# Kernel optimization log

Hardware: AMD Instinct MI355X
Metric: run time of the kernel (lower is better)

The kernel has to match this reference:

```python
import jax, jax.numpy as jnp
import numpy as np

HID = 256


def _mlp(h, ws, bs):
    # 4-layer MLP: tanh x3, sigmoid output (matches nn.Sequential in torch code)
    h = jnp.tanh(h @ ws[0] + bs[0])
    h = jnp.tanh(h @ ws[1] + bs[1])
    h = jnp.tanh(h @ ws[2] + bs[2])
    return jax.nn.sigmoid(h @ ws[3] + bs[3])


def setup_inputs() -> dict:
    key = jax.random.key(0)
    N, K, DE = 100000, 32, 8
    IN1 = K * DE          # 256
    MID = 5
    IN2 = K * MID         # 160
    E = N * K
    ks = jax.random.split(key, 20)
    x = jax.random.normal(ks[0], (N, DE), dtype=jnp.float32)
    edge_index = jax.random.randint(ks[1], (2, E), 0, N, dtype=jnp.int64)
    edge_attr = jax.random.normal(ks[2], (E, DE), dtype=jnp.float32)

    def lin(k, fan_in, fan_out):
        kw, kb = jax.random.split(k)
        lim = 1.0 / np.sqrt(fan_in)
        w = jax.random.uniform(kw, (fan_in, fan_out), jnp.float32, -lim, lim)
        b = jax.random.uniform(kb, (fan_out,), jnp.float32, -lim, lim)
        return w, b

    dims1 = [(IN1, HID), (HID, HID), (HID, HID), (HID, MID)]
    dims2 = [(IN2, HID), (HID, HID), (HID, HID), (HID, 1)]
    inp = {"x": x, "edge_index": edge_index, "edge_attr": edge_attr}
    for i, (fi, fo) in enumerate(dims1):
        w, b = lin(ks[3 + i], fi, fo)
        inp[f"w1_{i}"], inp[f"b1_{i}"] = w, b
    for i, (fi, fo) in enumerate(dims2):
        w, b = lin(ks[10 + i], fi, fo)
        inp[f"w2_{i}"], inp[f"b2_{i}"] = w, b
    return inp


def reference(x, edge_index, edge_attr,
              w1_0, b1_0, w1_1, b1_1, w1_2, b1_2, w1_3, b1_3,
              w2_0, b2_0, w2_1, b2_1, w2_2, b2_2, w2_3, b2_3):
    K = 32
    IN1 = w1_0.shape[0]              # 256
    MID = w1_3.shape[1]              # 5
    # GNN1: message = edge_attr; aggregate reshapes to [N, IN1] then MLP -> [N, MID]
    out1 = _mlp(edge_attr.reshape(-1, IN1), (w1_0, w1_1, w1_2, w1_3), (b1_0, b1_1, b1_2, b1_3))
    # GNN2: message = x_j = out1[edge_index[1]] (flow='target_to_source')
    gathered = out1[edge_index[1]]                     # [E, MID] irregular gather
    out2 = _mlp(gathered.reshape(-1, K * MID), (w2_0, w2_1, w2_2, w2_3), (b2_0, b2_1, b2_2, b2_3))
    return out2[:, 0]                                  # squeeze dim 1 -> [N]
```

## Files before the change

kernel.cpp:

```cpp
#include <hip/hip_runtime.h>
#include <stdint.h>

typedef uint16_t u16;
typedef uint32_t u32;
typedef __attribute__((ext_vector_type(8)))  __bf16 bf16x8;
typedef __attribute__((ext_vector_type(16))) float  f32x16;

#define NROWS   100000
#define E_EDGES 3200000

#define HIDX(r, g) (((r) << 8) + ((((g) ^ ((r) & 31))) << 3))

#define MFMA(a, b, c) __builtin_amdgcn_mfma_f32_32x32x16_bf16((a), (b), (c), 0, 0, 0)

__device__ __forceinline__ u32 pk_bf16(float a, float b) {
    u32 ua = __builtin_bit_cast(u32, a), ub = __builtin_bit_cast(u32, b);
    ua = (ua + 0x7FFFu + ((ua >> 16) & 1u)) >> 16;
    ub = (ub + 0x7FFFu + ((ub >> 16) & 1u)) >> 16;
    return ua | (ub << 16);
}
__device__ __forceinline__ float fast_tanh(float x) {
    float e = __expf(2.0f * x);
    return 1.0f - __fdividef(2.0f, e + 1.0f);
}
__device__ __forceinline__ float fast_sigmoid(float x) {
    return __fdividef(1.0f, 1.0f + __expf(-x));
}

__device__ __forceinline__ void dense256_reg(u16* Hs, const u16* __restrict__ WB,
                                             const float* __restrict__ bias,
                                             int wave, int lane) {
    const int l31 = lane & 31, lh = lane >> 5;
    const int nt0 = (wave & 3) * 2;
    const int bb  = (wave >> 2) * 2;
    const int rb0 = bb * 32 + l31, rb1 = rb0 + 32;

    f32x16 acc[4];
#pragma unroll
    for (int i = 0; i < 4; ++i)
#pragma unroll
        for (int j = 0; j < 16; ++j) acc[i][j] = 0.0f;

    __syncthreads();

    const u16* wbase = WB + (nt0 * 32 + l31) * 16 + lh * 8;
#pragma unroll
    for (int c = 0; c < 8; ++c) {
#pragma unroll
        for (int ks = 0; ks < 2; ++ks) {
            const int g = c * 4 + ks * 2 + lh;
            bf16x8 w0 = *(const bf16x8*)(wbase + c * 8192 + ks * 4096);
            bf16x8 w1 = *(const bf16x8*)(wbase + c * 8192 + ks * 4096 + 512);
            bf16x8 h0 = *(const bf16x8*)(Hs + HIDX(rb0, g));
            bf16x8 h1 = *(const bf16x8*)(Hs + HIDX(rb1, g));
            acc[0] = MFMA(w0, h0, acc[0]);
            acc[1] = MFMA(w0, h1, acc[1]);
            acc[2] = MFMA(w1, h0, acc[2]);
            acc[3] = MFMA(w1, h1, acc[3]);
        }
    }
    __syncthreads();

#pragma unroll
    for (int i = 0; i < 2; ++i) {
        const int nt = nt0 + i;
#pragma unroll
        for (int rg = 0; rg < 4; ++rg) {
            const int ns = nt * 32 + rg * 8 + lh * 4;
            const float4 bv = *(const float4*)(bias + ns);
#pragma unroll
            for (int b = 0; b < 2; ++b) {
                f32x16& A = acc[i * 2 + b];
                float x0 = fast_tanh(A[rg * 4 + 0] + bv.x);
                float x1 = fast_tanh(A[rg * 4 + 1] + bv.y);
                float x2 = fast_tanh(A[rg * 4 + 2] + bv.z);
                float x3 = fast_tanh(A[rg * 4 + 3] + bv.w);
                const int r = (bb + b) * 32 + l31;
                const int g = nt * 4 + rg;
                uint2 v; v.x = pk_bf16(x0, x1); v.y = pk_bf16(x2, x3);
                *(uint2*)(Hs + (r << 8) + (((g) ^ (r & 31)) << 3) + lh * 4) = v;
            }
        }
    }
}

__device__ __forceinline__ f32x16 final_dense_reg(const u16* Hs, const u16* __restrict__ WBf,
                                                  int wave, int lane) {
    const int l31 = lane & 31, lh = lane >> 5;
    __syncthreads();
    f32x16 acc;
#pragma unroll
    for (int j = 0; j < 16; ++j) acc[j] = 0.0f;
    if (wave < 4) {
        const u16* wbase = WBf + l31 * 16 + lh * 8;
#pragma unroll
        for (int c = 0; c < 8; ++c)
#pragma unroll
            for (int ks = 0; ks < 2; ++ks) {
                bf16x8 w = *(const bf16x8*)(wbase + (c * 2 + ks) * 512);
                const int g = c * 4 + ks * 2 + lh;
                bf16x8 h = *(const bf16x8*)(Hs + HIDX(wave * 32 + l31, g));
                acc = MFMA(w, h, acc);
            }
    }
    return acc;
}

__global__ __launch_bounds__(512, 4) void mlp1_kernel(
    const float* __restrict__ ea, const u16* __restrict__ WB1, const u16* __restrict__ WB13,
    const float* __restrict__ b0, const float* __restrict__ b1, const float* __restrict__ b2,
    const float* __restrict__ b3, u16* __restrict__ out1) {
    __shared__ u16 Hs[128 * 256];
    const int tid = threadIdx.x, wave = tid >> 6, lane = tid & 63, blk = blockIdx.x;

#pragma unroll
    for (int i = 0; i < 8; ++i) {
        const int r = i * 16 + (tid >> 5);
        const int g = tid & 31;
        const int rg_ = blk * 128 + r;
        if (rg_ < NROWS) {
            const float* p = ea + (size_t)rg_ * 256 + g * 8;
            float4 a0 = *(const float4*)p;
            float4 a1 = *(const float4*)(p + 4);
            uint4 v; v.x = pk_bf16(a0.x, a0.y); v.y = pk_bf16(a0.z, a0.w);
            v.z = pk_bf16(a1.x, a1.y); v.w = pk_bf16(a1.z, a1.w);
            *(uint4*)(Hs + HIDX(r, g)) = v;
        }
    }
    dense256_reg(Hs, WB1,          b0, wave, lane);
    dense256_reg(Hs, WB1 + 65536,  b1, wave, lane);
    dense256_reg(Hs, WB1 + 131072, b2, wave, lane);
    f32x16 acc = final_dense_reg(Hs, WB13, wave, lane);

    if (wave < 4) {
        const int row_g = blk * 128 + wave * 32 + (lane & 31);
        if (row_g < NROWS) {
            if ((lane >> 5) == 0) {
                float s0 = fast_sigmoid(acc[0] + b3[0]);
                float s1 = fast_sigmoid(acc[1] + b3[1]);
                float s2 = fast_sigmoid(acc[2] + b3[2]);
                float s3 = fast_sigmoid(acc[3] + b3[3]);
                uint2 v; v.x = pk_bf16(s0, s1); v.y = pk_bf16(s2, s3);
                *(uint2*)(out1 + (size_t)row_g * 8) = v;
            } else {
                float s4 = fast_sigmoid(acc[0] + b3[4]);
                uint2 v; v.x = pk_bf16(s4, 0.0f); v.y = 0u;
                *(uint2*)(out1 + (size_t)row_g * 8 + 4) = v;
            }
        }
    }
}

__global__ __launch_bounds__(512, 4) void mlp2_kernel(
    const int* __restrict__ idx1, const u16* __restrict__ out1,
    const u16* __restrict__ WB2, const u16* __restrict__ WB23,
    const float* __restrict__ b0, const float* __restrict__ b1, const float* __restrict__ b2,
    const float* __restrict__ b3, float* __restrict__ out) {
    __shared__ u16 Hs[128 * 256];
    const int tid = threadIdx.x, wave = tid >> 6, lane = tid & 63, blk = blockIdx.x;

    int nodes[8];
#pragma unroll
    for (int i = 0; i < 8; ++i) {
        const long e = (long)blk * 4096 + i * 512 + tid;
        nodes[i] = (e < (long)E_EDGES) ? idx1[e] : 0;
    }
#pragma unroll
    for (int i = 0; i < 8; ++i) {
        const int li = i * 512 + tid;
        const int r = li >> 5, j = li & 31;
        const long e = (long)blk * 4096 + li;
        if (e < (long)E_EDGES) {
            uint4 v = *(const uint4*)(out1 + (size_t)nodes[i] * 8);
            *(uint4*)(Hs + HIDX(r, j)) = v;
        }
    }
    dense256_reg(Hs, WB2,          b0, wave, lane);
    dense256_reg(Hs, WB2 + 65536,  b1, wave, lane);
    dense256_reg(Hs, WB2 + 131072, b2, wave, lane);
    f32x16 acc = final_dense_reg(Hs, WB23, wave, lane);

    if (wave < 4) {
        const int row_g = blk * 128 + wave * 32 + (lane & 31);
        if (row_g < NROWS && (lane >> 5) == 0)
            out[row_g] = fast_sigmoid(acc[0] + b3[0]);
    }
}

__global__ void transform_kernel(
    const float* __restrict__ w10, const float* __restrict__ w11, const float* __restrict__ w12,
    const float* __restrict__ w13, const float* __restrict__ w20, const float* __restrict__ w21,
    const float* __restrict__ w22, const float* __restrict__ w23, u16* __restrict__ ws) {
    const int id = blockIdx.x * 256 + threadIdx.x;
    float val;
    if (id < 196608) {
        int layer = id >> 16, rem = id & 65535;
        int c = rem >> 13, s = (rem >> 12) & 1, n = (rem >> 4) & 255, kl = rem & 15;
        int k = c * 32 + s * 16 + kl;
        const float* w = layer == 0 ? w10 : (layer == 1 ? w11 : w12);
        val = w[k * 256 + n];
    } else if (id < 204800) {
        int rem = id - 196608;
        int c = rem >> 10, s = (rem >> 9) & 1, n = (rem >> 4) & 31, kl = rem & 15;
        int k = c * 32 + s * 16 + kl;
        val = (n < 5) ? w13[k * 5 + n] : 0.0f;
    } else if (id < 401408) {
        int rem = id - 204800;
        int layer = rem >> 16; rem &= 65535;
        int c = rem >> 13, s = (rem >> 12) & 1, n = (rem >> 4) & 255, kl = rem & 15;
        int k = c * 32 + s * 16 + kl;
        if (layer == 0) {
            int j = k >> 3, v = k & 7;
            val = (v < 5) ? w20[(j * 5 + v) * 256 + n] : 0.0f;
        } else {
            val = (layer == 1 ? w21 : w22)[k * 256 + n];
        }
    } else {
        int rem = id - 401408;
        int c = rem >> 10, s = (rem >> 9) & 1, n = (rem >> 4) & 31, kl = rem & 15;
        int k = c * 32 + s * 16 + kl;
        val = (n == 0) ? w23[k] : 0.0f;
    }
    u32 u = __builtin_bit_cast(u32, val);
    u = (u + 0x7FFFu + ((u >> 16) & 1u)) >> 16;
    ws[id] = (u16)u;
}

extern "C" void kernel_launch(void* const* d_in, const int* in_sizes, int n_in,
                              void* d_out, int out_size, void* d_ws, size_t ws_size,
                              hipStream_t stream) {
    const int*   ei  = (const int*)d_in[1];
    const float* ea  = (const float*)d_in[2];
    const float* w10 = (const float*)d_in[3];  const float* b10 = (const float*)d_in[4];
    const float* w11 = (const float*)d_in[5];  const float* b11 = (const float*)d_in[6];
    const float* w12 = (const float*)d_in[7];  const float* b12 = (const float*)d_in[8];
    const float* w13 = (const float*)d_in[9];  const float* b13 = (const float*)d_in[10];
    const float* w20 = (const float*)d_in[11]; const float* b20 = (const float*)d_in[12];
    const float* w21 = (const float*)d_in[13]; const float* b21 = (const float*)d_in[14];
    const float* w22 = (const float*)d_in[15]; const float* b22 = (const float*)d_in[16];
    const float* w23 = (const float*)d_in[17]; const float* b23 = (const float*)d_in[18];

    u16* ws   = (u16*)d_ws;
    u16* WB1  = ws;
    u16* WB13 = ws + 196608;
    u16* WB2  = ws + 204800;
    u16* WB23 = ws + 401408;
    u16* out1 = ws + 409600;

    hipLaunchKernelGGL(transform_kernel, dim3(1600), dim3(256), 0, stream,
                       w10, w11, w12, w13, w20, w21, w22, w23, ws);
    hipLaunchKernelGGL(mlp1_kernel, dim3(782), dim3(512), 0, stream,
                       ea, WB1, WB13, b10, b11, b12, b13, out1);
    hipLaunchKernelGGL(mlp2_kernel, dim3(782), dim3(512), 0, stream,
                       ei + E_EDGES, out1, WB2, WB23, b20, b21, b22, b23, (float*)d_out);
}
```

Before: 396.0 us.

## Hold weight slices in registers, prefetch next layer, double-buffer activations in LDS

Each of the 8 waves now owns one 32-column output tile. It keeps its 16 weight fragments for the current layer in registers and overwrites them with the next layer's weights while the MFMA loop runs. Block row count drops from 128 to 64, with ping-pong LDS buffers H0/H1, so each layer needs one barrier instead of two and the grid doubles. This hides global weight-load latency behind compute and gives more blocks for occupancy. The cost is more register pressure and twice as many weight reads across blocks.

```diff
diff --git a/kernel.cpp b/kernel.cpp
--- a/kernel.cpp
+++ b/kernel.cpp
@@ -27,81 +27,59 @@
     return __fdividef(1.0f, 1.0f + __expf(-x));
 }
 
-__device__ __forceinline__ void dense256_reg(u16* Hs, const u16* __restrict__ WB,
-                                             const float* __restrict__ bias,
-                                             int wave, int lane) {
-    const int l31 = lane & 31, lh = lane >> 5;
-    const int nt0 = (wave & 3) * 2;
-    const int bb  = (wave >> 2) * 2;
-    const int rb0 = bb * 32 + l31, rb1 = rb0 + 32;
-
-    f32x16 acc[4];
-#pragma unroll
-    for (int i = 0; i < 4; ++i)
-#pragma unroll
-        for (int j = 0; j < 16; ++j) acc[i][j] = 0.0f;
-
-    __syncthreads();
-
-    const u16* wbase = WB + (nt0 * 32 + l31) * 16 + lh * 8;
-#pragma unroll
-    for (int c = 0; c < 8; ++c) {
-#pragma unroll
-        for (int ks = 0; ks < 2; ++ks) {
-            const int g = c * 4 + ks * 2 + lh;
-            bf16x8 w0 = *(const bf16x8*)(wbase + c * 8192 + ks * 4096);
-            bf16x8 w1 = *(const bf16x8*)(wbase + c * 8192 + ks * 4096 + 512);
-            bf16x8 h0 = *(const bf16x8*)(Hs + HIDX(rb0, g));
-            bf16x8 h1 = *(const bf16x8*)(Hs + HIDX(rb1, g));
-            acc[0] = MFMA(w0, h0, acc[0]);
-            acc[1] = MFMA(w0, h1, acc[1]);
-            acc[2] = MFMA(w1, h0, acc[2]);
-            acc[3] = MFMA(w1, h1, acc[3]);
-        }
-    }
-    __syncthreads();
-
-#pragma unroll
-    for (int i = 0; i < 2; ++i) {
-        const int nt = nt0 + i;
-#pragma unroll
-        for (int rg = 0; rg < 4; ++rg) {
-            const int ns = nt * 32 + rg * 8 + lh * 4;
-            const float4 bv = *(const float4*)(bias + ns);
-#pragma unroll
-            for (int b = 0; b < 2; ++b) {
-                f32x16& A = acc[i * 2 + b];
-                float x0 = fast_tanh(A[rg * 4 + 0] + bv.x);
-                float x1 = fast_tanh(A[rg * 4 + 1] + bv.y);
-                float x2 = fast_tanh(A[rg * 4 + 2] + bv.z);
-                float x3 = fast_tanh(A[rg * 4 + 3] + bv.w);
-                const int r = (bb + b) * 32 + l31;
-                const int g = nt * 4 + rg;
-                uint2 v; v.x = pk_bf16(x0, x1); v.y = pk_bf16(x2, x3);
-                *(uint2*)(Hs + (r << 8) + (((g) ^ (r & 31)) << 3) + lh * 4) = v;
-            }
-        }
-    }
-}
-
-__device__ __forceinline__ f32x16 final_dense_reg(const u16* Hs, const u16* __restrict__ WBf,
-                                                  int wave, int lane) {
-    const int l31 = lane & 31, lh = lane >> 5;
-    __syncthreads();
+__device__ __forceinline__ void load_w16(bf16x8 (&W)[16], const u16* __restrict__ base,
+                                         int stride) {
+#pragma unroll
+    for (int s = 0; s < 16; ++s) W[s] = *(const bf16x8*)(base + s * stride);
+}
+
+__device__ __forceinline__ void dense_layer(const u16* __restrict__ Hin, u16* __restrict__ Hout,
+                                            bf16x8 (&W)[16], const u16* __restrict__ pfbase,
+                                            int pfstride, const float* __restrict__ bias,
+                                            int nt, int l31, int lh) {
+    f32x16 acc0, acc1;
+#pragma unroll
+    for (int j = 0; j < 16; ++j) { acc0[j] = 0.0f; acc1[j] = 0.0f; }
+
+#pragma unroll
+    for (int s = 0; s < 16; ++s) {
+        const int g = 2 * s + lh;
+        bf16x8 h0 = *(const bf16x8*)(Hin + HIDX(l31, g));
+        bf16x8 h1 = *(const bf16x8*)(Hin + HIDX(32 + l31, g));
+        acc0 = MFMA(W[s], h0, acc0);
+        acc1 = MFMA(W[s], h1, acc1);
+        W[s] = *(const bf16x8*)(pfbase + s * pfstride);
+    }
+#pragma unroll
+    for (int rg = 0; rg < 4; ++rg) {
+        const float4 bv = *(const float4*)(bias + nt * 32 + rg * 8 + lh * 4);
+#pragma unroll
+        for (int b = 0; b < 2; ++b) {
+            const f32x16& A = b ? acc1 : acc0;
+            float x0 = fast_tanh(A[rg * 4 + 0] + bv.x);
+            float x1 = fast_tanh(A[rg * 4 + 1] + bv.y);
+            float x2 = fast_tanh(A[rg * 4 + 2] + bv.z);
+            float x3 = fast_tanh(A[rg * 4 + 3] + bv.w);
+            const int r = b * 32 + l31;
+            const int g = nt * 4 + rg;
+            uint2 v; v.x = pk_bf16(x0, x1); v.y = pk_bf16(x2, x3);
+            *(uint2*)(Hout + (r << 8) + (((g) ^ (r & 31)) << 3) + lh * 4) = v;
+        }
+    }
+}
+
+__device__ __forceinline__ f32x16 final_dense(const u16* __restrict__ Hin, bf16x8 (&W)[16],
+                                              int wave, int l31, int lh) {
     f32x16 acc;
 #pragma unroll
     for (int j = 0; j < 16; ++j) acc[j] = 0.0f;
-    if (wave < 4) {
-        const u16* wbase = WBf + l31 * 16 + lh * 8;
-#pragma unroll
-        for (int c = 0; c < 8; ++c)
-#pragma unroll
-            for (int ks = 0; ks < 2; ++ks) {
-                bf16x8 w = *(const bf16x8*)(wbase + (c * 2 + ks) * 512);
-                const int g = c * 4 + ks * 2 + lh;
-                bf16x8 h = *(const bf16x8*)(Hs + HIDX(wave * 32 + l31, g));
-                acc = MFMA(w, h, acc);
-            }
+    if (wave < 2) {
+#pragma unroll
+        for (int s = 0; s < 16; ++s) {
+            const int g = 2 * s + lh;
+            bf16x8 h = *(const bf16x8*)(Hin + HIDX(wave * 32 + l31, g));
+            acc = MFMA(W[s], h, acc);
+        }
     }
     return acc;
 }
@@ -110,32 +88,43 @@
     const float* __restrict__ ea, const u16* __restrict__ WB1, const u16* __restrict__ WB13,
     const float* __restrict__ b0, const float* __restrict__ b1, const float* __restrict__ b2,
     const float* __restrict__ b3, u16* __restrict__ out1) {
-    __shared__ u16 Hs[128 * 256];
+    __shared__ u16 H0[64 * 256];
+    __shared__ u16 H1[64 * 256];
     const int tid = threadIdx.x, wave = tid >> 6, lane = tid & 63, blk = blockIdx.x;
-
-#pragma unroll
-    for (int i = 0; i < 8; ++i) {
+    const int l31 = lane & 31, lh = lane >> 5, nt = wave;
+    const int woff = (nt * 32 + l31) * 16 + lh * 8;
+
+    bf16x8 W[16];
+    load_w16(W, WB1 + woff, 4096);
+
+#pragma unroll
+    for (int i = 0; i < 4; ++i) {
         const int r = i * 16 + (tid >> 5);
         const int g = tid & 31;
-        const int rg_ = blk * 128 + r;
+        const int rg_ = blk * 64 + r;
+        uint4 v = {0u, 0u, 0u, 0u};
         if (rg_ < NROWS) {
             const float* p = ea + (size_t)rg_ * 256 + g * 8;
             float4 a0 = *(const float4*)p;
             float4 a1 = *(const float4*)(p + 4);
-            uint4 v; v.x = pk_bf16(a0.x, a0.y); v.y = pk_bf16(a0.z, a0.w);
+            v.x = pk_bf16(a0.x, a0.y); v.y = pk_bf16(a0.z, a0.w);
             v.z = pk_bf16(a1.x, a1.y); v.w = pk_bf16(a1.z, a1.w);
-            *(uint4*)(Hs + HIDX(r, g)) = v;
-        }
-    }
-    dense256_reg(Hs, WB1,          b0, wave, lane);
-    dense256_reg(Hs, WB1 + 65536,  b1, wave, lane);
-    dense256_reg(Hs, WB1 + 131072, b2, wave, lane);
-    f32x16 acc = final_dense_reg(Hs, WB13, wave, lane);
-
-    if (wave < 4) {
-        const int row_g = blk * 128 + wave * 32 + (lane & 31);
+        }
+        *(uint4*)(H0 + HIDX(r, g)) = v;
+    }
+    __syncthreads();
+    dense_layer(H0, H1, W, WB1 + 65536  + woff, 4096, b0, nt, l31, lh);
+    __syncthreads();
+    dense_layer(H1, H0, W, WB1 + 131072 + woff, 4096, b1, nt, l31, lh);
+    __syncthreads();
+    dense_layer(H0, H1, W, WB13 + l31 * 16 + lh * 8, 512, b2, nt, l31, lh);
+    __syncthreads();
+    f32x16 acc = final_dense(H1, W, wave, l31, lh);
+
+    if (wave < 2) {
+        const int row_g = blk * 64 + wave * 32 + l31;
         if (row_g < NROWS) {
-            if ((lane >> 5) == 0) {
+            if (lh == 0) {
                 float s0 = fast_sigmoid(acc[0] + b3[0]);
                 float s1 = fast_sigmoid(acc[1] + b3[1]);
                 float s2 = fast_sigmoid(acc[2] + b3[2]);
@@ -156,33 +145,41 @@
     const u16* __restrict__ WB2, const u16* __restrict__ WB23,
     const float* __restrict__ b0, const float* __restrict__ b1, const float* __restrict__ b2,
     const float* __restrict__ b3, float* __restrict__ out) {
-    __shared__ u16 Hs[128 * 256];
+    __shared__ u16 H0[64 * 256];
+    __shared__ u16 H1[64 * 256];
     const int tid = threadIdx.x, wave = tid >> 6, lane = tid & 63, blk = blockIdx.x;
-
-    int nodes[8];
-#pragma unroll
-    for (int i = 0; i < 8; ++i) {
-        const long e = (long)blk * 4096 + i * 512 + tid;
-        nodes[i] = (e < (long)E_EDGES) ? idx1[e] : 0;
-    }
-#pragma unroll
-    for (int i = 0; i < 8; ++i) {
+    const int l31 = lane & 31, lh = lane >> 5, nt = wave;
+    const int woff = (nt * 32 + l31) * 16 + lh * 8;
+
+    bf16x8 W[16];
+    load_w16(W, WB2 + woff, 4096);
+
+    int nodes[4];
+#pragma unroll
+    for (int i = 0; i < 4; ++i) {
+        const long e = (long)blk * 2048 + i * 512 + tid;
+        nodes[i] = (e < (long)E_EDGES) ? idx1[e] : -1;
+    }
+#pragma unroll
+    for (int i = 0; i < 4; ++i) {
         const int li = i * 512 + tid;
         const int r = li >> 5, j = li & 31;
-        const long e = (long)blk * 4096 + li;
-        if (e < (long)E_EDGES) {
-            uint4 v = *(const uint4*)(out1 + (size_t)nodes[i] * 8);
-            *(uint4*)(Hs + HIDX(r, j)) = v;
-        }
-    }
-    dense256_reg(Hs, WB2,          b0, wave, lane);
-    dense256_reg(Hs, WB2 + 65536,  b1, wave, lane);
-    dense256_reg(Hs, WB2 + 131072, b2, wave, lane);
-    f32x16 acc = final_dense_reg(Hs, WB23, wave, lane);
-
-    if (wave < 4) {
-        const int row_g = blk * 128 + wave * 32 + (lane & 31);
-        if (row_g < NROWS && (lane >> 5) == 0)
+        uint4 v = {0u, 0u, 0u, 0u};
+        if (nodes[i] >= 0) v = *(const uint4*)(out1 + (size_t)nodes[i] * 8);
+        *(uint4*)(H0 + HIDX(r, j)) = v;
+    }
+    __syncthreads();
+    dense_layer(H0, H1, W, WB2 + 65536  + woff, 4096, b0, nt, l31, lh);
+    __syncthreads();
+    dense_layer(H1, H0, W, WB2 + 131072 + woff, 4096, b1, nt, l31, lh);
+    __syncthreads();
+    dense_layer(H0, H1, W, WB23 + l31 * 16 + lh * 8, 512, b2, nt, l31, lh);
+    __syncthreads();
+    f32x16 acc = final_dense(H1, W, wave, l31, lh);
+
+    if (wave < 2) {
+        const int row_g = blk * 64 + wave * 32 + l31;
+        if (row_g < NROWS && lh == 0)
             out[row_g] = fast_sigmoid(acc[0] + b3[0]);
     }
 }
@@ -249,8 +246,8 @@
 
     hipLaunchKernelGGL(transform_kernel, dim3(1600), dim3(256), 0, stream,
                        w10, w11, w12, w13, w20, w21, w22, w23, ws);
-    hipLaunchKernelGGL(mlp1_kernel, dim3(782), dim3(512), 0, stream,
+    hipLaunchKernelGGL(mlp1_kernel, dim3(1563), dim3(512), 0, stream,
                        ea, WB1, WB13, b10, b11, b12, b13, out1);
-    hipLaunchKernelGGL(mlp2_kernel, dim3(782), dim3(512), 0, stream,
+    hipLaunchKernelGGL(mlp2_kernel, dim3(1563), dim3(512), 0, stream,
                        ei + E_EDGES, out1, WB2, WB23, b20, b21, b22, b23, (float*)d_out);
 }
```

Measured after the change: 364.2 us. -8.0%, faster.

## Shrink row tile to 64 with 4-wave blocks, software-pipeline MFMA loads

Applied to the files above, without the earlier changes.

Blocks now handle 64 rows with 256 threads instead of 128 rows with 512. Each wave computes 64 output columns for all 64 rows, so the weight layout is reordered to a plain K-step stride. The MFMA inner loop double-buffers its weight and LDS operand loads so they overlap the previous step's MFMAs. tanh and sigmoid now use the hardware exp2 and rcp builtins. The smaller tile halves LDS use and raises grid size, which should improve occupancy and load balance. The cost is that each weight fragment is reused across fewer rows.

```diff
diff --git a/kernel.cpp b/kernel.cpp
--- a/kernel.cpp
+++ b/kernel.cpp
@@ -13,28 +13,25 @@
 
 #define MFMA(a, b, c) __builtin_amdgcn_mfma_f32_32x32x16_bf16((a), (b), (c), 0, 0, 0)
 
-__device__ __forceinline__ u32 pk_bf16(float a, float b) {
+__device__ __forceinline__ u32 pk2(float a, float b) {
     u32 ua = __builtin_bit_cast(u32, a), ub = __builtin_bit_cast(u32, b);
     ua = (ua + 0x7FFFu + ((ua >> 16) & 1u)) >> 16;
     ub = (ub + 0x7FFFu + ((ub >> 16) & 1u)) >> 16;
     return ua | (ub << 16);
 }
 __device__ __forceinline__ float fast_tanh(float x) {
-    float e = __expf(2.0f * x);
-    return 1.0f - __fdividef(2.0f, e + 1.0f);
+    float e = __builtin_amdgcn_exp2f(x * 2.885390081777927f);
+    float r = __builtin_amdgcn_rcpf(e + 1.0f);
+    return __builtin_fmaf(-2.0f, r, 1.0f);
 }
 __device__ __forceinline__ float fast_sigmoid(float x) {
-    return __fdividef(1.0f, 1.0f + __expf(-x));
-}
-
-__device__ __forceinline__ void dense256_reg(u16* Hs, const u16* __restrict__ WB,
-                                             const float* __restrict__ bias,
-                                             int wave, int lane) {
-    const int l31 = lane & 31, lh = lane >> 5;
-    const int nt0 = (wave & 3) * 2;
-    const int bb  = (wave >> 2) * 2;
-    const int rb0 = bb * 32 + l31, rb1 = rb0 + 32;
-
+    float e = __builtin_amdgcn_exp2f(x * -1.4426950408889634f);
+    return __builtin_amdgcn_rcpf(1.0f + e);
+}
+
+__device__ __forceinline__ void dense256(u16* __restrict__ Hs, const u16* __restrict__ WB,
+                                         const float* __restrict__ bias,
+                                         int wave, int l31, int lh) {
     f32x16 acc[4];
 #pragma unroll
     for (int i = 0; i < 4; ++i)
@@ -43,146 +40,155 @@
 
     __syncthreads();
 
-    const u16* wbase = WB + (nt0 * 32 + l31) * 16 + lh * 8;
-#pragma unroll
-    for (int c = 0; c < 8; ++c) {
-#pragma unroll
-        for (int ks = 0; ks < 2; ++ks) {
-            const int g = c * 4 + ks * 2 + lh;
-            bf16x8 w0 = *(const bf16x8*)(wbase + c * 8192 + ks * 4096);
-            bf16x8 w1 = *(const bf16x8*)(wbase + c * 8192 + ks * 4096 + 512);
-            bf16x8 h0 = *(const bf16x8*)(Hs + HIDX(rb0, g));
-            bf16x8 h1 = *(const bf16x8*)(Hs + HIDX(rb1, g));
-            acc[0] = MFMA(w0, h0, acc[0]);
-            acc[1] = MFMA(w0, h1, acc[1]);
-            acc[2] = MFMA(w1, h0, acc[2]);
-            acc[3] = MFMA(w1, h1, acc[3]);
-        }
+    const u16* wp = WB + (wave * 64 + l31) * 16 + lh * 8;
+    bf16x8 w0 = *(const bf16x8*)(wp);
+    bf16x8 w1 = *(const bf16x8*)(wp + 512);
+    bf16x8 h0 = *(const bf16x8*)(Hs + HIDX(l31, lh));
+    bf16x8 h1 = *(const bf16x8*)(Hs + HIDX(32 + l31, lh));
+
+#pragma unroll
+    for (int s = 0; s < 16; ++s) {
+        bf16x8 nw0 = w0, nw1 = w1, nh0 = h0, nh1 = h1;
+        if (s < 15) {
+            const int ng = 2 * (s + 1) + lh;
+            nw0 = *(const bf16x8*)(wp + (s + 1) * 4096);
+            nw1 = *(const bf16x8*)(wp + (s + 1) * 4096 + 512);
+            nh0 = *(const bf16x8*)(Hs + HIDX(l31, ng));
+            nh1 = *(const bf16x8*)(Hs + HIDX(32 + l31, ng));
+        }
+        acc[0] = MFMA(w0, h0, acc[0]);
+        acc[1] = MFMA(w0, h1, acc[1]);
+        acc[2] = MFMA(w1, h0, acc[2]);
+        acc[3] = MFMA(w1, h1, acc[3]);
+        w0 = nw0; w1 = nw1; h0 = nh0; h1 = nh1;
     }
     __syncthreads();
 
 #pragma unroll
     for (int i = 0; i < 2; ++i) {
-        const int nt = nt0 + i;
+        const int nt = wave * 2 + i;
 #pragma unroll
         for (int rg = 0; rg < 4; ++rg) {
-            const int ns = nt * 32 + rg * 8 + lh * 4;
-            const float4 bv = *(const float4*)(bias + ns);
+            const float4 bv = *(const float4*)(bias + nt * 32 + rg * 8 + lh * 4);
 #pragma unroll
             for (int b = 0; b < 2; ++b) {
-                f32x16& A = acc[i * 2 + b];
+                const f32x16& A = acc[i * 2 + b];
                 float x0 = fast_tanh(A[rg * 4 + 0] + bv.x);
                 float x1 = fast_tanh(A[rg * 4 + 1] + bv.y);
                 float x2 = fast_tanh(A[rg * 4 + 2] + bv.z);
                 float x3 = fast_tanh(A[rg * 4 + 3] + bv.w);
-                const int r = (bb + b) * 32 + l31;
+                const int r = b * 32 + l31;
                 const int g = nt * 4 + rg;
-                uint2 v; v.x = pk_bf16(x0, x1); v.y = pk_bf16(x2, x3);
+                uint2 v; v.x = pk2(x0, x1); v.y = pk2(x2, x3);
                 *(uint2*)(Hs + (r << 8) + (((g) ^ (r & 31)) << 3) + lh * 4) = v;
             }
         }
     }
 }
 
-__device__ __forceinline__ f32x16 final_dense_reg(const u16* Hs, const u16* __restrict__ WBf,
-                                                  int wave, int lane) {
-    const int l31 = lane & 31, lh = lane >> 5;
+__device__ __forceinline__ f32x16 final_dense(const u16* __restrict__ Hs,
+                                              const u16* __restrict__ WBf,
+                                              int wave, int l31, int lh) {
     __syncthreads();
     f32x16 acc;
 #pragma unroll
     for (int j = 0; j < 16; ++j) acc[j] = 0.0f;
-    if (wave < 4) {
-        const u16* wbase = WBf + l31 * 16 + lh * 8;
-#pragma unroll
-        for (int c = 0; c < 8; ++c)
-#pragma unroll
-            for (int ks = 0; ks < 2; ++ks) {
-                bf16x8 w = *(const bf16x8*)(wbase + (c * 2 + ks) * 512);
-                const int g = c * 4 + ks * 2 + lh;
-                bf16x8 h = *(const bf16x8*)(Hs + HIDX(wave * 32 + l31, g));
-                acc = MFMA(w, h, acc);
+    if (wave < 2) {
+        const u16* wp = WBf + l31 * 16 + lh * 8;
+        bf16x8 w = *(const bf16x8*)(wp);
+        bf16x8 h = *(const bf16x8*)(Hs + HIDX(wave * 32 + l31, lh));
+#pragma unroll
+        for (int s = 0; s < 16; ++s) {
+            bf16x8 nw = w, nh = h;
+            if (s < 15) {
+                nw = *(const bf16x8*)(wp + (s + 1) * 512);
+                nh = *(const bf16x8*)(Hs + HIDX(wave * 32 + l31, 2 * (s + 1) + lh));
             }
+            acc = MFMA(w, h, acc);
+            w = nw; h = nh;
+        }
     }
     return acc;
 }
 
-__global__ __launch_bounds__(512, 4) void mlp1_kernel(
+__global__ __launch_bounds__(256, 4) void mlp1_kernel(
     const float* __restrict__ ea, const u16* __restrict__ WB1, const u16* __restrict__ WB13,
     const float* __restrict__ b0, const float* __restrict__ b1, const float* __restrict__ b2,
     const float* __restrict__ b3, u16* __restrict__ out1) {
-    __shared__ u16 Hs[128 * 256];
+    __shared__ u16 Hs[64 * 256];
     const int tid = threadIdx.x, wave = tid >> 6, lane = tid & 63, blk = blockIdx.x;
+    const int l31 = lane & 31, lh = lane >> 5;
 
 #pragma unroll
     for (int i = 0; i < 8; ++i) {
-        const int r = i * 16 + (tid >> 5);
-        const int g = tid & 31;
-        const int rg_ = blk * 128 + r;
+        const int li = i * 256 + tid;
+        const int r = li >> 5, g = li & 31;
+        const int rg_ = blk * 64 + r;
+        uint4 v = {0u, 0u, 0u, 0u};
         if (rg_ < NROWS) {
             const float* p = ea + (size_t)rg_ * 256 + g * 8;
             float4 a0 = *(const float4*)p;
             float4 a1 = *(const float4*)(p + 4);
-            uint4 v; v.x = pk_bf16(a0.x, a0.y); v.y = pk_bf16(a0.z, a0.w);
-            v.z = pk_bf16(a1.x, a1.y); v.w = pk_bf16(a1.z, a1.w);
-            *(uint4*)(Hs + HIDX(r, g)) = v;
-        }
-    }
-    dense256_reg(Hs, WB1,          b0, wave, lane);
-    dense256_reg(Hs, WB1 + 65536,  b1, wave, lane);
-    dense256_reg(Hs, WB1 + 131072, b2, wave, lane);
-    f32x16 acc = final_dense_reg(Hs, WB13, wave, lane);
-
-    if (wave < 4) {
-        const int row_g = blk * 128 + wave * 32 + (lane & 31);
+            v.x = pk2(a0.x, a0.y); v.y = pk2(a0.z, a0.w);
+            v.z = pk2(a1.x, a1.y); v.w = pk2(a1.z, a1.w);
+        }
+        *(uint4*)(Hs + HIDX(r, g)) = v;
+    }
+    dense256(Hs, WB1,          b0, wave, l31, lh);
+    dense256(Hs, WB1 + 65536,  b1, wave, l31, lh);
+    dense256(Hs, WB1 + 131072, b2, wave, l31, lh);
+    f32x16 acc = final_dense(Hs, WB13, wave, l31, lh);
+
+    if (wave < 2) {
+        const int row_g = blk * 64 + wave * 32 + l31;
         if (row_g < NROWS) {
-            if ((lane >> 5) == 0) {
+            if (lh == 0) {
                 float s0 = fast_sigmoid(acc[0] + b3[0]);
                 float s1 = fast_sigmoid(acc[1] + b3[1]);
                 float s2 = fast_sigmoid(acc[2] + b3[2]);
                 float s3 = fast_sigmoid(acc[3] + b3[3]);
-                uint2 v; v.x = pk_bf16(s0, s1); v.y = pk_bf16(s2, s3);
+                uint2 v; v.x = pk2(s0, s1); v.y = pk2(s2, s3);
                 *(uint2*)(out1 + (size_t)row_g * 8) = v;
             } else {
                 float s4 = fast_sigmoid(acc[0] + b3[4]);
-                uint2 v; v.x = pk_bf16(s4, 0.0f); v.y = 0u;
+                uint2 v; v.x = pk2(s4, 0.0f); v.y = 0u;
                 *(uint2*)(out1 + (size_t)row_g * 8 + 4) = v;
             }
         }
     }
 }
 
-__global__ __launch_bounds__(512, 4) void mlp2_kernel(
+__global__ __launch_bounds__(256, 4) void mlp2_kernel(
     const int* __restrict__ idx1, const u16* __restrict__ out1,
     const u16* __restrict__ WB2, const u16* __restrict__ WB23,
     const float* __restrict__ b0, const float* __restrict__ b1, const float* __restrict__ b2,
     const float* __restrict__ b3, float* __restrict__ out) {
-    __shared__ u16 Hs[128 * 256];
+    __shared__ u16 Hs[64 * 256];
     const int tid = threadIdx.x, wave = tid >> 6, lane = tid & 63, blk = blockIdx.x;
+    const int l31 = lane & 31, lh = lane >> 5;
 
     int nodes[8];
 #pragma unroll
     for (int i = 0; i < 8; ++i) {
-        const long e = (long)blk * 4096 + i * 512 + tid;
-        nodes[i] = (e < (long)E_EDGES) ? idx1[e] : 0;
+        const long e = (long)blk * 2048 + i * 256 + tid;
+        nodes[i] = (e < (long)E_EDGES) ? idx1[e] : -1;
     }
 #pragma unroll
     for (int i = 0; i < 8; ++i) {
-        const int li = i * 512 + tid;
+        const int li = i * 256 + tid;
         const int r = li >> 5, j = li & 31;
-        const long e = (long)blk * 4096 + li;
-        if (e < (long)E_EDGES) {
-            uint4 v = *(const uint4*)(out1 + (size_t)nodes[i] * 8);
-            *(uint4*)(Hs + HIDX(r, j)) = v;
-        }
-    }
-    dense256_reg(Hs, WB2,          b0, wave, lane);
-    dense256_reg(Hs, WB2 + 65536,  b1, wave, lane);
-    dense256_reg(Hs, WB2 + 131072, b2, wave, lane);
-    f32x16 acc = final_dense_reg(Hs, WB23, wave, lane);
-
-    if (wave < 4) {
-        const int row_g = blk * 128 + wave * 32 + (lane & 31);
-        if (row_g < NROWS && (lane >> 5) == 0)
+        uint4 v = {0u, 0u, 0u, 0u};
+        if (nodes[i] >= 0) v = *(const uint4*)(out1 + (size_t)nodes[i] * 8);
+        *(uint4*)(Hs + HIDX(r, j)) = v;
+    }
+    dense256(Hs, WB2,          b0, wave, l31, lh);
+    dense256(Hs, WB2 + 65536,  b1, wave, l31, lh);
+    dense256(Hs, WB2 + 131072, b2, wave, l31, lh);
+    f32x16 acc = final_dense(Hs, WB23, wave, l31, lh);
+
+    if (wave < 2) {
+        const int row_g = blk * 64 + wave * 32 + l31;
+        if (row_g < NROWS && lh == 0)
             out[row_g] = fast_sigmoid(acc[0] + b3[0]);
     }
 }
@@ -195,20 +201,20 @@
     float val;
     if (id < 196608) {
         int layer = id >> 16, rem = id & 65535;
-        int c = rem >> 13, s = (rem >> 12) & 1, n = (rem >> 4) & 255, kl = rem & 15;
-        int k = c * 32 + s * 16 + kl;
+        int s = rem >> 12, n = (rem >> 4) & 255, kl = rem & 15;
+        int k = s * 16 + kl;
         const float* w = layer == 0 ? w10 : (layer == 1 ? w11 : w12);
         val = w[k * 256 + n];
     } else if (id < 204800) {
         int rem = id - 196608;
-        int c = rem >> 10, s = (rem >> 9) & 1, n = (rem >> 4) & 31, kl = rem & 15;
-        int k = c * 32 + s * 16 + kl;
+        int s = rem >> 9, n = (rem >> 4) & 31, kl = rem & 15;
+        int k = s * 16 + kl;
         val = (n < 5) ? w13[k * 5 + n] : 0.0f;
     } else if (id < 401408) {
         int rem = id - 204800;
         int layer = rem >> 16; rem &= 65535;
-        int c = rem >> 13, s = (rem >> 12) & 1, n = (rem >> 4) & 255, kl = rem & 15;
-        int k = c * 32 + s * 16 + kl;
+        int s = rem >> 12, n = (rem >> 4) & 255, kl = rem & 15;
+        int k = s * 16 + kl;
         if (layer == 0) {
             int j = k >> 3, v = k & 7;
             val = (v < 5) ? w20[(j * 5 + v) * 256 + n] : 0.0f;
@@ -217,8 +223,8 @@
         }
     } else {
         int rem = id - 401408;
-        int c = rem >> 10, s = (rem >> 9) & 1, n = (rem >> 4) & 31, kl = rem & 15;
-        int k = c * 32 + s * 16 + kl;
+        int s = rem >> 9, n = (rem >> 4) & 31, kl = rem & 15;
+        int k = s * 16 + kl;
         val = (n == 0) ? w23[k] : 0.0f;
     }
     u32 u = __builtin_bit_cast(u32, val);
@@ -249,8 +255,8 @@
 
     hipLaunchKernelGGL(transform_kernel, dim3(1600), dim3(256), 0, stream,
                        w10, w11, w12, w13, w20, w21, w22, w23, ws);
-    hipLaunchKernelGGL(mlp1_kernel, dim3(782), dim3(512), 0, stream,
+    hipLaunchKernelGGL(mlp1_kernel, dim3(1563), dim3(256), 0, stream,
                        ea, WB1, WB13, b10, b11, b12, b13, out1);
-    hipLaunchKernelGGL(mlp2_kernel, dim3(782), dim3(512), 0, stream,
+    hipLaunchKernelGGL(mlp2_kernel, dim3(1563), dim3(256), 0, stream,
                        ei + E_EDGES, out1, WB2, WB23, b20, b21, b22, b23, (float*)d_out);
 }
```

New measurement: 332.9 us. 1.19x faster.
